# Performance work log

Measured on AMD Instinct MI355X. Metric: run time of the kernel, lower is better.

## Reference

```python
import jax, jax.numpy as jnp
import numpy as np

EPS_COV = 0.01  # module eps added to covariance diagonal
G, N_MEM = 8, 64  # groups, channels per group


def _pade_coeffs(m=5):
    # Taylor coefficients of sqrt(1 - x): c_k = (-1)^k * binom(1/2, k)
    c = np.zeros(2 * m + 1)
    c[0] = 1.0
    b = 1.0
    for k in range(1, 2 * m + 1):
        b *= (0.5 - (k - 1)) / k
        c[k] = ((-1) ** k) * b
    # Pade [m/m]: q_0 = 1, solve sum_j q_j c_{k-j} = 0 for k = m+1..2m
    A = np.zeros((m, m))
    rhs = np.zeros(m)
    for i in range(m):
        k = m + 1 + i
        for j in range(m):
            A[i, j] = c[k - (j + 1)]
        rhs[i] = -c[k]
    q = np.concatenate([[1.0], np.linalg.solve(A, rhs)])
    p = np.array([sum(q[j] * c[k - j] for j in range(min(k, m) + 1)) for k in range(m + 1)])
    return p, q

_PADE_P, _PADE_Q = _pade_coeffs(5)


def matrix_pade_approximant(p, I):
    # evaluates the [5/5] Pade approximant of sqrt at p (normalized SPD matrix)
    pp = jnp.asarray(_PADE_P, dtype=p.dtype)
    pq = jnp.asarray(_PADE_Q, dtype=p.dtype)
    p_app = I - p
    p_sqrt = pp[0] * I
    q_sqrt = pq[0] * I
    p_hat = p_app
    for i in range(5):
        p_sqrt = p_sqrt + pp[i + 1] * p_hat
        q_sqrt = q_sqrt + pq[i + 1] * p_hat
        p_hat = p_hat @ p_app
    return jnp.linalg.solve(q_sqrt, p_sqrt)


def mpa_sqrt(M):
    # batched matrix square root via Pade approximant (MPA_Lya.forward)
    normM = jnp.linalg.norm(M, axis=(1, 2))[:, None, None]
    n = M.shape[1]
    I = jnp.broadcast_to(jnp.eye(n, dtype=M.dtype), M.shape)
    return matrix_pade_approximant(M / normM, I) * jnp.sqrt(normM)


def setup_inputs() -> dict:
    key = jax.random.key(0)
    k1, k2 = jax.random.split(key)
    x = jax.random.normal(k1, (32, 512, 64, 64), dtype=jnp.float32)
    weight = jax.random.uniform(k2, (G, N_MEM, 1), dtype=jnp.float32)
    bias = jnp.zeros((G, N_MEM, 1), dtype=jnp.float32)
    return {"x": x, "weight": weight, "bias": bias}


def reference(x, weight, bias):
    N, C, H, W = x.shape
    n_mem = C // G
    xg = jnp.transpose(x, (1, 0, 2, 3)).reshape(G, n_mem, -1)  # (G, n_mem, N*H*W)
    mu = jnp.mean(xg, axis=2, keepdims=True)
    xg = xg - mu
    I = jnp.eye(n_mem, dtype=x.dtype)[None]
    xxt = jnp.einsum('gim,gjm->gij', xg, xg) / (N * H * W) + I * EPS_COV
    subspace = jnp.linalg.inv(mpa_sqrt(xxt))  # ZCA whitening matrix per group
    xr = jnp.einsum('gij,gjm->gim', subspace, xg)
    xr = xr * weight + bias
    xr = xr.reshape(C, N, H, W)
    return jnp.transpose(xr, (1, 0, 2, 3))
```

## Files before the change

### kernel.cpp

```cpp
#include <hip/hip_runtime.h>

#define NBATCH 32
#define CHAN   512
#define HWSZ   4096
#define NG     8
#define NM     64
#define MTOT   (NBATCH * HWSZ)
#define EPSC   0.01f
#define P68    68

typedef _Float16 f16;
typedef _Float16 f16x8 __attribute__((ext_vector_type(8)));
typedef float    f32x4 __attribute__((ext_vector_type(4)));

#define MFMA16(a, b, c) __builtin_amdgcn_mfma_f32_16x16x32_f16(a, b, c, 0, 0, 0)

__global__ __launch_bounds__(256) void gram_k(const float* __restrict__ x,
                                              float* __restrict__ gpart,
                                              float* __restrict__ spart) {
    __shared__ __align__(16) f16 tile[64 * 128];
    __shared__ float red[2][4096];

    const int bid  = blockIdx.x;
    const int g    = bid >> 6;
    const int n    = (bid >> 1) & 31;
    const int half = bid & 1;
    const float* xb = x + ((size_t)(n * CHAN + g * NM)) * HWSZ + half * 2048;

    const int t = threadIdx.x;
    const int w = t >> 6;
    const int l = t & 63;

    f32x4 acc[4][4];
#pragma unroll
    for (int i = 0; i < 4; ++i)
#pragma unroll
        for (int j = 0; j < 4; ++j) acc[i][j] = (f32x4){0.f, 0.f, 0.f, 0.f};
    float fsum[4] = {0.f, 0.f, 0.f, 0.f};

    for (int tt = 0; tt < 16; ++tt) {
        const float* xt = xb + tt * 128;
#pragma unroll
        for (int i = 0; i < 4; ++i) {
            const int p    = t + 256 * i;
            const int ch   = p >> 4;
            const int off8 = (p & 15) * 8;
            const float4 v0 = *(const float4*)(xt + (size_t)ch * HWSZ + off8);
            const float4 v1 = *(const float4*)(xt + (size_t)ch * HWSZ + off8 + 4);
            fsum[i] += (v0.x + v0.y) + (v0.z + v0.w) + (v1.x + v1.y) + (v1.z + v1.w);
            f16x8 hv;
            hv[0] = (f16)v0.x; hv[1] = (f16)v0.y; hv[2] = (f16)v0.z; hv[3] = (f16)v0.w;
            hv[4] = (f16)v1.x; hv[5] = (f16)v1.y; hv[6] = (f16)v1.z; hv[7] = (f16)v1.w;
            *(f16x8*)&tile[ch * 128 + (off8 ^ ((ch & 7) << 3))] = hv;
        }
        __syncthreads();

        f16x8 frag[4];
#pragma unroll
        for (int rb = 0; rb < 4; ++rb) {
            const int ch = rb * 16 + (l & 15);
            const int k0 = w * 32 + (l >> 4) * 8;
            frag[rb] = *(const f16x8*)&tile[ch * 128 + (k0 ^ ((ch & 7) << 3))];
        }
#pragma unroll
        for (int i = 0; i < 4; ++i)
#pragma unroll
            for (int j = 0; j < 4; ++j)
                acc[i][j] = MFMA16(frag[i], frag[j], acc[i][j]);
        __syncthreads();
    }

#pragma unroll
    for (int i = 0; i < 4; ++i) {
        fsum[i] += __shfl_xor(fsum[i], 1);
        fsum[i] += __shfl_xor(fsum[i], 2);
        fsum[i] += __shfl_xor(fsum[i], 4);
        fsum[i] += __shfl_xor(fsum[i], 8);
    }
    if ((l & 15) == 0) {
        const int chb = t >> 4;
#pragma unroll
        for (int i = 0; i < 4; ++i)
            spart[(size_t)bid * 64 + chb + 16 * i] = fsum[i];
    }

    if (w >= 2) {
#pragma unroll
        for (int i = 0; i < 4; ++i)
#pragma unroll
            for (int j = 0; j < 4; ++j)
#pragma unroll
                for (int r = 0; r < 4; ++r) {
                    const int row = i * 16 + (l >> 4) * 4 + r;
                    const int col = j * 16 + (l & 15);
                    red[w - 2][row * 64 + col] = acc[i][j][r];
                }
    }
    __syncthreads();
    if (w < 2) {
#pragma unroll
        for (int i = 0; i < 4; ++i)
#pragma unroll
            for (int j = 0; j < 4; ++j)
#pragma unroll
                for (int r = 0; r < 4; ++r) {
                    const int row = i * 16 + (l >> 4) * 4 + r;
                    const int col = j * 16 + (l & 15);
                    red[w][row * 64 + col] += acc[i][j][r];
                }
    }
    __syncthreads();
#pragma unroll
    for (int k = 0; k < 16; ++k) {
        const int e = t + 256 * k;
        gpart[(size_t)bid * 4096 + e] = red[0][e] + red[1][e];
    }
}

__global__ __launch_bounds__(256) void solve_k(const float* __restrict__ gpart,
                                               const float* __restrict__ spart,
                                               const float* __restrict__ wgt,
                                               const float* __restrict__ bias,
                                               f16* __restrict__ Tf,
                                               float* __restrict__ offv) {
    __shared__ __align__(16) float A[64 * P68];
    __shared__ __align__(16) float B[64 * P68];
    __shared__ __align__(16) float Cc[64 * P68];
    __shared__ __align__(16) float Dd[64 * P68];
    __shared__ float mus[64];
    __shared__ float red[4];
    __shared__ float tr16[16];

    const int g = blockIdx.x, t = threadIdx.x;

    float covv[16], cov2[16];
#pragma unroll
    for (int k = 0; k < 16; ++k) { covv[k] = 0.f; cov2[k] = 0.f; }
    for (int p = 0; p < 64; p += 2) {
        const float* gp0 = gpart + ((size_t)(g * 64 + p)) * 4096;
        const float* gp1 = gp0 + 4096;
#pragma unroll
        for (int k = 0; k < 16; ++k) {
            covv[k] += gp0[t + 256 * k];
            cov2[k] += gp1[t + 256 * k];
        }
    }
#pragma unroll
    for (int k = 0; k < 16; ++k) covv[k] += cov2[k];

    if (t < 64) {
        float ss = 0.f;
#pragma unroll 8
        for (int p = 0; p < 64; ++p) ss += spart[(size_t)(g * 64 + p) * 64 + t];
        mus[t] = ss * (1.0f / MTOT);
    }
    __syncthreads();

    float loc = 0.f;
#pragma unroll
    for (int k = 0; k < 16; ++k) {
        const int e = t + 256 * k;
        const int i = e >> 6, j = e & 63;
        const float cv = covv[k] * (1.0f / MTOT) - mus[i] * mus[j] + (i == j ? EPSC : 0.f);
        covv[k] = cv;
        loc += cv * cv;
    }
#pragma unroll
    for (int o = 32; o > 0; o >>= 1) loc += __shfl_down(loc, o);
    if ((t & 63) == 0) red[t >> 6] = loc;
    __syncthreads();
    const float normM = sqrtf(red[0] + red[1] + red[2] + red[3]);
    const float ninv  = 1.0f / normM;

#pragma unroll
    for (int k = 0; k < 16; ++k) {
        const int e = t + 256 * k;
        const int i = e >> 6, j = e & 63;
        const float pa = (i == j ? 1.f : 0.f) - covv[k] * ninv;
        A[i * P68 + j] = pa;
        B[i * P68 + j] = pa;
    }
    __syncthreads();

    const int ty = t >> 4, tx = t & 15;
    const int i0 = ty * 4, j0 = tx * 4;

    const float PP[6] = {1.f, -2.75f, 2.75f, -1.203125f, 0.21484375f, -0.0107421875f};
    const float QQ[6] = {1.f, -2.25f, 1.75f, -0.546875f, 0.05859375f, -0.0009765625f};

    float pacc[4][4], qacc[4][4];
#pragma unroll
    for (int ai = 0; ai < 4; ++ai)
#pragma unroll
        for (int bi = 0; bi < 4; ++bi) {
            const int i = i0 + ai, j = j0 + bi;
            const float pa = A[i * P68 + j];
            const float id = (i == j) ? 1.f : 0.f;
            pacc[ai][bi] = PP[0] * id + PP[1] * pa;
            qacc[ai][bi] = QQ[0] * id + QQ[1] * pa;
        }

    float* src = B;
    float* dst = Cc;
    for (int s = 0; s < 4; ++s) {
        float mm[4][4];
#pragma unroll
        for (int ai = 0; ai < 4; ++ai)
#pragma unroll
            for (int bi = 0; bi < 4; ++bi) mm[ai][bi] = 0.f;
        for (int kk = 0; kk < 64; ++kk) {
            const float4 a4 = *(const float4*)&src[kk * P68 + i0];
            const float4 b4 = *(const float4*)&A[kk * P68 + j0];
            const float av[4] = {a4.x, a4.y, a4.z, a4.w};
            const float bv[4] = {b4.x, b4.y, b4.z, b4.w};
#pragma unroll
            for (int ai = 0; ai < 4; ++ai)
#pragma unroll
                for (int bi = 0; bi < 4; ++bi)
                    mm[ai][bi] = fmaf(av[ai], bv[bi], mm[ai][bi]);
        }
#pragma unroll
        for (int ai = 0; ai < 4; ++ai) {
            float4 w4;
            w4.x = mm[ai][0]; w4.y = mm[ai][1]; w4.z = mm[ai][2]; w4.w = mm[ai][3];
            *(float4*)&dst[(i0 + ai) * P68 + j0] = w4;
        }
#pragma unroll
        for (int ai = 0; ai < 4; ++ai)
#pragma unroll
            for (int bi = 0; bi < 4; ++bi) {
                pacc[ai][bi] = fmaf(PP[s + 2], mm[ai][bi], pacc[ai][bi]);
                qacc[ai][bi] = fmaf(QQ[s + 2], mm[ai][bi], qacc[ai][bi]);
            }
        __syncthreads();
        float* tmpp = src; src = dst; dst = tmpp;
    }

    if (ty == tx)
        tr16[tx] = pacc[0][0] + pacc[1][1] + pacc[2][2] + pacc[3][3];
    __syncthreads();
    float trsum = 0.f;
#pragma unroll
    for (int i = 0; i < 16; ++i) trsum += tr16[i];
    const float cP  = trsum * (1.0f / 64.0f);
    const float icP = 1.0f / cP;

#pragma unroll
    for (int ai = 0; ai < 4; ++ai) {
        float4 we, wq;
        const int i = i0 + ai;
        we.x = pacc[ai][0] * icP - (i == j0 + 0 ? 1.f : 0.f);
        we.y = pacc[ai][1] * icP - (i == j0 + 1 ? 1.f : 0.f);
        we.z = pacc[ai][2] * icP - (i == j0 + 2 ? 1.f : 0.f);
        we.w = pacc[ai][3] * icP - (i == j0 + 3 ? 1.f : 0.f);
        wq.x = qacc[ai][0]; wq.y = qacc[ai][1]; wq.z = qacc[ai][2]; wq.w = qacc[ai][3];
        *(float4*)&A[i * P68 + j0] = we;
        *(float4*)&B[i * P68 + j0] = wq;
    }
    __syncthreads();

    float* rsrc = B;
    float* rdst = Cc;
    for (int it = 0; it < 4; ++it) {
        float mm[4][4];
#pragma unroll
        for (int ai = 0; ai < 4; ++ai)
#pragma unroll
            for (int bi = 0; bi < 4; ++bi) mm[ai][bi] = 0.f;
        for (int kk = 0; kk < 64; ++kk) {
            const float4 a4 = *(const float4*)&A[kk * P68 + i0];
            const float4 b4 = *(const float4*)&rsrc[kk * P68 + j0];
            const float av[4] = {a4.x, a4.y, a4.z, a4.w};
            const float bv[4] = {b4.x, b4.y, b4.z, b4.w};
#pragma unroll
            for (int ai = 0; ai < 4; ++ai)
#pragma unroll
                for (int bi = 0; bi < 4; ++bi)
                    mm[ai][bi] = fmaf(av[ai], bv[bi], mm[ai][bi]);
        }
#pragma unroll
        for (int ai = 0; ai < 4; ++ai) {
            const float4 q4 = *(const float4*)&B[(i0 + ai) * P68 + j0];
            float4 w4;
            w4.x = q4.x - mm[ai][0]; w4.y = q4.y - mm[ai][1];
            w4.z = q4.z - mm[ai][2]; w4.w = q4.w - mm[ai][3];
            *(float4*)&rdst[(i0 + ai) * P68 + j0] = w4;
        }
        __syncthreads();
        if (it == 0) { rsrc = Cc; rdst = Dd; }
        else { float* tmpp = rsrc; rsrc = rdst; rdst = tmpp; }
    }
    float* X = rsrc;

    const float invs = icP / sqrtf(normM);
    if (t < 64) {
        float sm = 0.f;
        for (int j = 0; j < 64; ++j) sm += X[t * P68 + j] * mus[j];
        offv[g * NM + t] = bias[g * NM + t] - sm * invs * wgt[g * NM + t];
    }
#pragma unroll
    for (int k = 0; k < 16; ++k) {
        const int e = t + 256 * k;
        const int i = e >> 6, j = e & 63;
        Tf[(size_t)g * 4096 + e] = (f16)(X[i * P68 + j] * invs * wgt[g * NM + i]);
    }
}

__global__ __launch_bounds__(256) void apply_k(const float* __restrict__ x,
                                               const f16* __restrict__ Tf,
                                               const float* __restrict__ offv,
                                               float* __restrict__ out) {
    __shared__ __align__(16) f16 xs[128 * 64];
    __shared__ __align__(16) f16 Ts[4096];
    __shared__ float offs[64];

    const int bid  = 511 - (int)blockIdx.x;
    const int g    = bid >> 6;
    const int n    = (bid >> 1) & 31;
    const int half = bid & 1;
    const size_t base = ((size_t)(n * CHAN + g * NM)) * HWSZ + half * 2048;
    const float* xb = x + base;
    float* ob = out + base;

    const int t = threadIdx.x;
    const int w = t >> 6;
    const int l = t & 63;

#pragma unroll
    for (int i = 0; i < 2; ++i) {
        const int c   = t + 256 * i;
        const int oc  = c >> 3;
        const int icb = (c & 7) * 8;
        const f16x8 v = *(const f16x8*)&Tf[(size_t)g * 4096 + oc * 64 + icb];
        *(f16x8*)&Ts[oc * 64 + (icb ^ ((oc & 7) << 3))] = v;
    }
    if (t < 64) offs[t] = offv[g * NM + t];
    __syncthreads();

    f16x8 afrag[2];
#pragma unroll
    for (int c = 0; c < 2; ++c) {
        const int oc = w * 16 + (l & 15);
        const int k0 = c * 32 + (l >> 4) * 8;
        afrag[c] = *(const f16x8*)&Ts[oc * 64 + (k0 ^ ((oc & 7) << 3))];
    }
    float offr[4];
#pragma unroll
    for (int r = 0; r < 4; ++r) offr[r] = offs[w * 16 + (l >> 4) * 4 + r];

    for (int tt = 15; tt >= 0; --tt) {
        const float* xt = xb + tt * 128;
        __syncthreads();
#pragma unroll
        for (int i = 0; i < 4; ++i) {
            const int p    = t + 256 * i;
            const int ch   = p >> 4;
            const int off8 = (p & 15) * 8;
            const float4 v0 = *(const float4*)(xt + (size_t)ch * HWSZ + off8);
            const float4 v1 = *(const float4*)(xt + (size_t)ch * HWSZ + off8 + 4);
            f16 h[8];
            h[0] = (f16)v0.x; h[1] = (f16)v0.y; h[2] = (f16)v0.z; h[3] = (f16)v0.w;
            h[4] = (f16)v1.x; h[5] = (f16)v1.y; h[6] = (f16)v1.z; h[7] = (f16)v1.w;
#pragma unroll
            for (int j = 0; j < 8; ++j) {
                const int pos = off8 + j;
                xs[pos * 64 + (ch ^ (((pos ^ (pos >> 3)) & 7) << 3))] = h[j];
            }
        }
        __syncthreads();

#pragma unroll
        for (int pb = 0; pb < 8; ++pb) {
            f32x4 acc;
            acc[0] = offr[0]; acc[1] = offr[1]; acc[2] = offr[2]; acc[3] = offr[3];
            const int pos = pb * 16 + (l & 15);
            const int swz = ((pos ^ (pos >> 3)) & 7) << 3;
#pragma unroll
            for (int c = 0; c < 2; ++c) {
                const int k0 = c * 32 + (l >> 4) * 8;
                const f16x8 bfrag = *(const f16x8*)&xs[pos * 64 + (k0 ^ swz)];
                acc = MFMA16(afrag[c], bfrag, acc);
            }
            const int posg = tt * 128 + pb * 16 + (l & 15);
#pragma unroll
            for (int r = 0; r < 4; ++r) {
                const int oc = w * 16 + (l >> 4) * 4 + r;
                __builtin_nontemporal_store(acc[r], &ob[(size_t)oc * HWSZ + posg]);
            }
        }
    }
}

extern "C" void kernel_launch(void* const* d_in, const int* in_sizes, int n_in,
                              void* d_out, int out_size, void* d_ws, size_t ws_size,
                              hipStream_t stream) {
    const float* x    = (const float*)d_in[0];
    const float* wgt  = (const float*)d_in[1];
    const float* bias = (const float*)d_in[2];
    float* out = (float*)d_out;

    float* ws    = (float*)d_ws;
    float* gpart = ws;
    float* spart = ws + 2097152;
    float* offv  = ws + 2129920;
    f16*   Tf    = (f16*)(ws + 2130432);

    gram_k <<<512, 256, 0, stream>>>(x, gpart, spart);
    solve_k<<<8,   256, 0, stream>>>(gpart, spart, wgt, bias, Tf, offv);
    apply_k<<<512, 256, 0, stream>>>(x, Tf, offv, out);
}
```

Measured before the change: 215.8 us.

## Stash f16 copy of input in gram pass and reuse it in apply

The gram kernel now also writes the f16-converted input tile to a workspace buffer in a contiguous per-block layout, and reads x with nontemporal loads. The apply kernel reads this half-precision buffer instead of re-reading and converting the fp32 input. This halves the bytes apply reads, but adds a 134 MB write in the gram pass, so total DRAM traffic is roughly unchanged unless the f16 buffer hits in cache.

```diff
diff --git a/kernel.cpp b/kernel.cpp
--- a/kernel.cpp
+++ b/kernel.cpp
@@ -12,12 +12,14 @@
 typedef _Float16 f16;
 typedef _Float16 f16x8 __attribute__((ext_vector_type(8)));
 typedef float    f32x4 __attribute__((ext_vector_type(4)));
+typedef float    fvec4 __attribute__((ext_vector_type(4)));
 
 #define MFMA16(a, b, c) __builtin_amdgcn_mfma_f32_16x16x32_f16(a, b, c, 0, 0, 0)
 
 __global__ __launch_bounds__(256) void gram_k(const float* __restrict__ x,
                                               float* __restrict__ gpart,
-                                              float* __restrict__ spart) {
+                                              float* __restrict__ spart,
+                                              f16* __restrict__ xh) {
     __shared__ __align__(16) f16 tile[64 * 128];
     __shared__ float red[2][4096];
 
@@ -40,18 +42,22 @@
 
     for (int tt = 0; tt < 16; ++tt) {
         const float* xt = xb + tt * 128;
+        f16* xht = xh + ((size_t)(bid * 16 + tt) * 1024) * 8;
 #pragma unroll
         for (int i = 0; i < 4; ++i) {
             const int p    = t + 256 * i;
             const int ch   = p >> 4;
             const int off8 = (p & 15) * 8;
-            const float4 v0 = *(const float4*)(xt + (size_t)ch * HWSZ + off8);
-            const float4 v1 = *(const float4*)(xt + (size_t)ch * HWSZ + off8 + 4);
+            const fvec4 v0 = __builtin_nontemporal_load(
+                (const fvec4*)(xt + (size_t)ch * HWSZ + off8));
+            const fvec4 v1 = __builtin_nontemporal_load(
+                (const fvec4*)(xt + (size_t)ch * HWSZ + off8 + 4));
             fsum[i] += (v0.x + v0.y) + (v0.z + v0.w) + (v1.x + v1.y) + (v1.z + v1.w);
             f16x8 hv;
             hv[0] = (f16)v0.x; hv[1] = (f16)v0.y; hv[2] = (f16)v0.z; hv[3] = (f16)v0.w;
             hv[4] = (f16)v1.x; hv[5] = (f16)v1.y; hv[6] = (f16)v1.z; hv[7] = (f16)v1.w;
             *(f16x8*)&tile[ch * 128 + (off8 ^ ((ch & 7) << 3))] = hv;
+            *(f16x8*)&xht[(size_t)p * 8] = hv;
         }
         __syncthreads();
 
@@ -306,7 +312,7 @@
     }
 }
 
-__global__ __launch_bounds__(256) void apply_k(const float* __restrict__ x,
+__global__ __launch_bounds__(256) void apply_k(const f16* __restrict__ xh,
                                                const f16* __restrict__ Tf,
                                                const float* __restrict__ offv,
                                                float* __restrict__ out) {
@@ -318,9 +324,7 @@
     const int g    = bid >> 6;
     const int n    = (bid >> 1) & 31;
     const int half = bid & 1;
-    const size_t base = ((size_t)(n * CHAN + g * NM)) * HWSZ + half * 2048;
-    const float* xb = x + base;
-    float* ob = out + base;
+    float* ob = out + ((size_t)(n * CHAN + g * NM)) * HWSZ + half * 2048;
 
     const int t = threadIdx.x;
     const int w = t >> 6;
@@ -349,22 +353,18 @@
     for (int r = 0; r < 4; ++r) offr[r] = offs[w * 16 + (l >> 4) * 4 + r];
 
     for (int tt = 15; tt >= 0; --tt) {
-        const float* xt = xb + tt * 128;
+        const f16* xt = xh + ((size_t)(bid * 16 + tt) * 1024) * 8;
         __syncthreads();
 #pragma unroll
         for (int i = 0; i < 4; ++i) {
             const int p    = t + 256 * i;
             const int ch   = p >> 4;
             const int off8 = (p & 15) * 8;
-            const float4 v0 = *(const float4*)(xt + (size_t)ch * HWSZ + off8);
-            const float4 v1 = *(const float4*)(xt + (size_t)ch * HWSZ + off8 + 4);
-            f16 h[8];
-            h[0] = (f16)v0.x; h[1] = (f16)v0.y; h[2] = (f16)v0.z; h[3] = (f16)v0.w;
-            h[4] = (f16)v1.x; h[5] = (f16)v1.y; h[6] = (f16)v1.z; h[7] = (f16)v1.w;
+            const f16x8 v = *(const f16x8*)&xt[(size_t)p * 8];
 #pragma unroll
             for (int j = 0; j < 8; ++j) {
                 const int pos = off8 + j;
-                xs[pos * 64 + (ch ^ (((pos ^ (pos >> 3)) & 7) << 3))] = h[j];
+                xs[pos * 64 + (ch ^ (((pos ^ (pos >> 3)) & 7) << 3))] = v[j];
             }
         }
         __syncthreads();
@@ -404,8 +404,9 @@
     float* spart = ws + 2097152;
     float* offv  = ws + 2129920;
     f16*   Tf    = (f16*)(ws + 2130432);
-
-    gram_k <<<512, 256, 0, stream>>>(x, gpart, spart);
+    f16*   xh    = (f16*)(ws + 2146816);
+
+    gram_k <<<512, 256, 0, stream>>>(x, gpart, spart, xh);
     solve_k<<<8,   256, 0, stream>>>(gpart, spart, wgt, bias, Tf, offv);
-    apply_k<<<512, 256, 0, stream>>>(x, Tf, offv, out);
+    apply_k<<<512, 256, 0, stream>>>(xh, Tf, offv, out);
 }
```

After: 229.2 us. 6.2% more time.
